# Performance work log

Hardware: AMD Instinct MI355X
Metric: run time of the kernel (lower is better)

## Reference

```python
import jax, jax.numpy as jnp
import numpy as np

B, L, D, T, NL = 64, 512, 512, 5000, 2


def setup_inputs() -> dict:
    key = jax.random.key(0)
    k1, k2, k3, k4 = jax.random.split(key, 4)
    enc_output = jax.random.normal(k1, (B, L, D), dtype=jnp.float32)
    # stands in for the row/col-normalized tag co-occurrence matrix (values in [0, 0.01])
    ui_adj = jax.random.uniform(k2, (T, T), dtype=jnp.float32) * 0.01
    # one GCN weight matrix per layer in the layer_stack
    Ws = jax.random.normal(k3, (NL, D, D), dtype=jnp.float32) / np.sqrt(D).astype(np.float32)
    # event ids are 1-indexed in the original (it indexes with e - 1)
    event_type = jax.random.randint(k4, (B, L), 1, T + 1, dtype=jnp.int64)
    slf_attn_mask = jnp.zeros((B, L, L), dtype=bool)
    non_pad_mask = jnp.ones((B, L), dtype=bool)
    return {"enc_output": enc_output, "ui_adj": ui_adj, "Ws": Ws,
            "event_type": event_type, "slf_attn_mask": slf_attn_mask,
            "non_pad_mask": non_pad_mask}


def reference(enc_output, ui_adj, Ws, event_type, slf_attn_mask, non_pad_mask):
    # --- batched per-sample adjacency gather (replaces the Python loop) ---
    idx = event_type - 1                                   # [B, L] 0-indexed
    sub = ui_adj[idx[:, :, None], idx[:, None, :]]         # [B, L, L] = ui_adj[e-1,:][:, e-1]
    diag = ui_adj[idx, idx]                                # [B, L]   = ui_adj[e-1, e-1]
    adj = sub + diag[:, None, :]                           # vector broadcasts across rows, as in torch
    # --- GNN layer stack (hGCN layer ~ relu(A @ X @ W)) ---
    x = enc_output
    for l in range(Ws.shape[0]):                           # small fixed n_layers loop
        x = jax.nn.relu(jnp.einsum('bij,bjd->bid', adj, x) @ Ws[l])
    # --- mean pool over sequence ---
    return x.mean(axis=1)                                  # [B, D]
```

## Files before the change

kernel.cpp:

```cpp
#include <hip/hip_runtime.h>

typedef unsigned short u16;
typedef unsigned int u32;
typedef __bf16 bf16x8 __attribute__((ext_vector_type(8)));
typedef float f32x4 __attribute__((ext_vector_type(4)));
typedef int i32x4 __attribute__((ext_vector_type(4)));
typedef u32 u32x2 __attribute__((ext_vector_type(2)));
typedef u32 u32x4 __attribute__((ext_vector_type(4)));

#define T_ 5000
#define CAP 96

__device__ __forceinline__ u16 f2bf(float f) {
  u32 u = __float_as_uint(f);
  u += 0x7fffu + ((u >> 16) & 1u);
  return (u16)(u >> 16);
}
__device__ __forceinline__ float bf2f(u32 bits16) {
  return __uint_as_float(bits16 << 16);
}

__device__ __forceinline__ void gload_lds16(const u16* g, u16* l) {
  __builtin_amdgcn_global_load_lds(
      (__attribute__((address_space(1))) void*)(u16*)g,
      (__attribute__((address_space(3))) void*)l, 16, 0, 0);
}

__device__ __forceinline__ u32 lds_off(const void* p) {
  return (u32)(uintptr_t)(__attribute__((address_space(3))) const void*)p;
}

__global__ void transpose_cast(const float* __restrict__ src, u16* __restrict__ dst) {
  __shared__ float tile[32][33];
  const int tx = threadIdx.x, ty = threadIdx.y;
  const int a0 = blockIdx.x * 32;
  const int b0 = blockIdx.y * 32;
  const size_t zoff = (size_t)blockIdx.z * (512 * 512);
  const float* s = src + zoff;
  u16* d = dst + zoff;
#pragma unroll
  for (int r = 0; r < 4; ++r)
    tile[ty + r * 8][tx] = s[(size_t)(a0 + ty + r * 8) * 512 + b0 + tx];
  __syncthreads();
#pragma unroll
  for (int r = 0; r < 4; ++r)
    d[(size_t)(b0 + ty + r * 8) * 512 + a0 + tx] = f2bf(tile[tx][ty + r * 8]);
}

__global__ void zero_k(int* __restrict__ cnt) {
  const int t = blockIdx.x * 256 + threadIdx.x;
  if (t < 5001) cnt[t] = 0;
}

__global__ void fill_k(const int* __restrict__ ev, const float* __restrict__ ui,
                       int2* __restrict__ cd, int* __restrict__ cnt,
                       int* __restrict__ list, int* __restrict__ ovf) {
  const int t = blockIdx.x * 256 + threadIdx.x;
  const int r = ev[t] - 1;
  int2 v;
  v.x = r;
  v.y = __float_as_int(ui[(size_t)r * (T_ + 1)]);
  cd[t] = v;
  const int pos = atomicAdd(&cnt[r], 1);
  if (pos < CAP) list[r * CAP + pos] = t;
  else { const int o = atomicAdd(&cnt[5000], 1); ovf[o] = t; }
}

__global__ __launch_bounds__(256)
void grow_gather(const float* __restrict__ ui, const int2* __restrict__ cd,
                 const int* __restrict__ cnt, const int* __restrict__ list,
                 u16* __restrict__ adj) {
  const int r = blockIdx.x;
  int c = cnt[r];
  if (c <= 0) return;
  if (c > CAP) c = CAP;
  __shared__ float row[5000];
  const float* __restrict__ src = ui + (size_t)r * T_;
  for (int t = threadIdx.x; t < 1250; t += 256)
    *(float4*)&row[t * 4] = *(const float4*)&src[t * 4];
  __syncthreads();
  const int j = threadIdx.x * 2;
  const int lb = r * CAP;
  int q = 0;
  for (; q + 2 <= c; q += 2) {
    const int t0 = list[lb + q], t1 = list[lb + q + 1];
    const int b0 = (t0 >> 9) << 9, b1 = (t1 >> 9) << 9;
    const int4 p0 = *(const int4*)&cd[b0 + j];
    const int4 p1 = *(const int4*)&cd[b1 + j];
    const u32 pk0 = (u32)f2bf(row[p0.x] + __int_as_float(p0.y)) |
                    ((u32)f2bf(row[p0.z] + __int_as_float(p0.w)) << 16);
    const u32 pk1 = (u32)f2bf(row[p1.x] + __int_as_float(p1.y)) |
                    ((u32)f2bf(row[p1.z] + __int_as_float(p1.w)) << 16);
    *(u32*)&adj[(size_t)t0 * 512 + j] = pk0;
    *(u32*)&adj[(size_t)t1 * 512 + j] = pk1;
  }
  if (q < c) {
    const int t0 = list[lb + q];
    const int b0 = (t0 >> 9) << 9;
    const int4 p0 = *(const int4*)&cd[b0 + j];
    const u32 pk0 = (u32)f2bf(row[p0.x] + __int_as_float(p0.y)) |
                    ((u32)f2bf(row[p0.z] + __int_as_float(p0.w)) << 16);
    *(u32*)&adj[(size_t)t0 * 512 + j] = pk0;
  }
}

__global__ void ovf_gather(const float* __restrict__ ui, const int2* __restrict__ cd,
                           const int* __restrict__ cnt, const int* __restrict__ ovf,
                           u16* __restrict__ adj) {
  const int n = cnt[5000];
  for (int q = blockIdx.x; q < n; q += gridDim.x) {
    const int t = ovf[q];
    const int base = (t >> 9) << 9;
    const long r = (long)cd[t].x;
    const float* __restrict__ row = ui + r * (long)T_;
    const int j = threadIdx.x * 2;
    const int4 p = *(const int4*)&cd[base + j];
    const u32 pk = (u32)f2bf(row[p.x] + __int_as_float(p.y)) |
                   ((u32)f2bf(row[p.z] + __int_as_float(p.w)) << 16);
    *(u32*)&adj[(size_t)t * 512 + j] = pk;
  }
}

template <int MODE, int BSRC>
__global__ __launch_bounds__(512, 2)
void gemm256(const u16* __restrict__ A, const void* __restrict__ Bv,
             u16* __restrict__ C, size_t strideA, size_t strideB, size_t strideC,
             float* __restrict__ P) {
  extern __shared__ u16 smem[];
  const int tid = threadIdx.x;
  const int lane = tid & 63;
  const int w = tid >> 6;
  const int wm = w >> 2, wn = w & 3;
  const int chunk = gridDim.x >> 3;
  const int wg = blockIdx.x;
  const int mapped = (wg & 7) * chunk + (wg >> 3);
  const int batch = mapped >> 2;
  const int tm = (mapped >> 1) & 1, tn = mapped & 1;
  const int m0 = tm << 8, n0 = tn << 8;
  const u16* __restrict__ Ab = A + (size_t)batch * strideA;

  const u16* gA[2];
  u32 ldA[2];
#pragma unroll
  for (int r = 0; r < 2; ++r) {
    const int c = r * 512 + tid;
    const int L = c * 16;
    const int pp = L >> 7;
    const int off = (L & 127) ^ ((pp & 7) << 4);
    const int m = pp * 2 + (off >> 6);
    const int kb = off & 63;
    gA[r] = Ab + (size_t)(m0 + m) * 512 + (kb >> 1);
    ldA[r] = (u32)((r * 512 + w * 64) * 8);
  }

  const u16* gB[2] = {nullptr, nullptr};
  u32 ldB[2] = {0, 0};
  if (BSRC == 0) {
    const u16* __restrict__ Bb = (const u16*)Bv + (size_t)batch * strideB;
#pragma unroll
    for (int r = 0; r < 2; ++r) {
      const int c = r * 512 + tid;
      const int L = c * 16;
      const int pp = L >> 7;
      const int off = (L & 127) ^ ((pp & 7) << 4);
      const int m = pp * 2 + (off >> 6);
      const int kb = off & 63;
      gB[r] = Bb + (size_t)(n0 + m) * 512 + (kb >> 1);
      ldB[r] = (u32)(32768 + (r * 512 + w * 64) * 8);
    }
  }

  const int dp = tid & 127;
  const int lq = tid >> 7;
  unsigned long long encB = 0;
  u32 boff0 = 0;
  u32x2 bs0[8], bs1[8];
  if (BSRC == 1) {
    encB = (unsigned long long)(uintptr_t)((const float*)Bv + (size_t)batch * strideB);
    boff0 = (u32)(((lq * 8) * 512 + n0 + dp * 2) * 4);
  }

#define BLOAD(t, S)                                                          \
  {                                                                          \
    const u32 ob = boff0 + (u32)(t) * 65536u;                                \
    _Pragma("unroll") for (int i = 0; i < 8; ++i)                            \
        asm volatile("global_load_dwordx2 %0, %1, %2"                        \
                     : "=v"(S[i])                                            \
                     : "v"(ob + (u32)i * 2048u), "s"(encB));                 \
  }

#define CONVERT_B(S)                                                         \
  {                                                                          \
    u32 wrd0[4], wrd1[4];                                                    \
    _Pragma("unroll") for (int jj = 0; jj < 4; ++jj) {                       \
      asm("v_cvt_pk_bf16_f32 %0, %1, %2"                                     \
          : "=v"(wrd0[jj]) : "v"(S[2 * jj].x), "v"(S[2 * jj + 1].x));        \
      asm("v_cvt_pk_bf16_f32 %0, %1, %2"                                     \
          : "=v"(wrd1[jj]) : "v"(S[2 * jj].y), "v"(S[2 * jj + 1].y));        \
    }                                                                        \
    const u32 by0 = (u32)dp * 128u + ((((u32)lq * 16u)) ^ (((u32)dp & 7u) << 4)); \
    const u32 by1 = (u32)dp * 128u + ((64u | ((u32)lq * 16u)) ^ (((u32)dp & 7u) << 4)); \
    u32x4 v0, v1;                                                            \
    v0.x = wrd0[0]; v0.y = wrd0[1]; v0.z = wrd0[2]; v0.w = wrd0[3];          \
    v1.x = wrd1[0]; v1.y = wrd1[1]; v1.z = wrd1[2]; v1.w = wrd1[3];          \
    *(u32x4*)((char*)smem + 65536 + by0) = v0;                               \
    *(u32x4*)((char*)smem + 65536 + by1) = v1;                               \
  }

  const int lr = lane & 15;
  const int kb = (lane >> 4) << 4;
  u32 aOff[8], bOff[4];
#pragma unroll
  for (int m = 0; m < 8; ++m) {
    const int row = wm * 128 + m * 16 + lr;
    aOff[m] = (u32)((row >> 1) * 128 + ((((row & 1) << 6) | kb) ^ (((row >> 1) & 7) << 4)));
  }
#pragma unroll
  for (int n = 0; n < 4; ++n) {
    const int row = wn * 64 + n * 16 + lr;
    bOff[n] = (u32)(65536 + (row >> 1) * 128 + ((((row & 1) << 6) | kb) ^ (((row >> 1) & 7) << 4)));
  }
  const u32 ldsBase = lds_off(smem);

  f32x4 acc[8][4] = {};

  auto stageA = [&](int t) {
    const u32 bo = (u32)(t & 3) * 8192;
#pragma unroll
    for (int r = 0; r < 2; ++r) gload_lds16(gA[r] + t * 32, smem + bo + ldA[r]);
  };
  auto stageB0 = [&](int t) {
    const u32 bo = (u32)(t & 3) * 8192;
#pragma unroll
    for (int r = 0; r < 2; ++r) gload_lds16(gB[r] + t * 32, smem + bo + ldB[r]);
  };

  if (BSRC == 0) {
    stageA(0); stageB0(0); stageA(1); stageB0(1); stageA(2); stageB0(2);
  } else {
    stageA(0); stageA(1); stageA(2);
    BLOAD(0, bs0); BLOAD(1, bs1);
  }

#pragma unroll
  for (int t = 0; t < 16; ++t) {
    if (BSRC == 0) {
      if (t <= 13)      asm volatile("s_waitcnt vmcnt(8)" ::: "memory");
      else if (t == 14) asm volatile("s_waitcnt vmcnt(4)" ::: "memory");
      else              asm volatile("s_waitcnt vmcnt(0)" ::: "memory");
      __builtin_amdgcn_sched_barrier(0);
      if (t + 3 < 16) { stageA(t + 3); stageB0(t + 3); }
      asm volatile("" ::: "memory");
      __builtin_amdgcn_s_barrier();
      asm volatile("" ::: "memory");
    } else {
      if (t == 0)              asm volatile("s_waitcnt vmcnt(8)" ::: "memory");
      else if (t <= 13)        asm volatile("s_waitcnt vmcnt(10)" ::: "memory");
      else if (t == 14)        asm volatile("s_waitcnt vmcnt(8)" ::: "memory");
      else                     asm volatile("s_waitcnt vmcnt(0)" ::: "memory");
      __builtin_amdgcn_sched_barrier(0);
      if (t & 1) { CONVERT_B(bs1); } else { CONVERT_B(bs0); }
      if (t + 3 < 16) stageA(t + 3);
      if (t + 2 < 16) { if (t & 1) { BLOAD(t + 2, bs1); } else { BLOAD(t + 2, bs0); } }
      asm volatile("s_waitcnt lgkmcnt(0)" ::: "memory");
      __builtin_amdgcn_s_barrier();
      asm volatile("" ::: "memory");
    }

    const u32 abase = ldsBase + (u32)(t & 3) * 16384;
    const u32 bbase = (BSRC == 0) ? (ldsBase + (u32)(t & 3) * 16384) : ldsBase;
    i32x4 araw[8], braw[4];
#pragma unroll
    for (int m = 0; m < 8; ++m)
      asm volatile("ds_read_b128 %0, %1" : "=v"(araw[m]) : "v"(abase + aOff[m]));
#pragma unroll
    for (int n = 0; n < 4; ++n)
      asm volatile("ds_read_b128 %0, %1" : "=v"(braw[n]) : "v"(bbase + bOff[n]));
    asm volatile("s_waitcnt lgkmcnt(0)" ::: "memory");
    __builtin_amdgcn_sched_barrier(0);

    __builtin_amdgcn_s_setprio(1);
#pragma unroll
    for (int m = 0; m < 8; ++m)
#pragma unroll
      for (int n = 0; n < 4; ++n)
        acc[m][n] = __builtin_amdgcn_mfma_f32_16x16x32_bf16(
            __builtin_bit_cast(bf16x8, araw[m]),
            __builtin_bit_cast(bf16x8, braw[n]), acc[m][n], 0, 0, 0);
    __builtin_amdgcn_s_setprio(0);
    asm volatile("" ::: "memory");
    __builtin_amdgcn_s_barrier();
    __builtin_amdgcn_sched_barrier(0);
  }
#undef BLOAD
#undef CONVERT_B

  u16* Cb = C + (size_t)batch * strideC;
  if (MODE == 0) {
#pragma unroll
    for (int m = 0; m < 8; ++m) {
      const int row = m0 + wm * 128 + m * 16 + (lane >> 4) * 4;
#pragma unroll
      for (int n = 0; n < 4; ++n) {
        const int col = n0 + wn * 64 + n * 16 + (lane & 15);
        const f32x4 v = acc[m][n];
#pragma unroll
        for (int j = 0; j < 4; ++j)
          Cb[(size_t)(row + j) * 512 + col] = f2bf(v[j]);
      }
    }
  } else if (MODE == 1) {
#pragma unroll
    for (int m = 0; m < 8; ++m) {
      const int i = m0 + wm * 128 + m * 16 + (lane >> 4) * 4;
#pragma unroll
      for (int n = 0; n < 4; ++n) {
        const int d = n0 + wn * 64 + n * 16 + (lane & 15);
        const f32x4 v = acc[m][n];
        uint2 p;
        p.x = (u32)f2bf(fmaxf(v[0], 0.f)) | ((u32)f2bf(fmaxf(v[1], 0.f)) << 16);
        p.y = (u32)f2bf(fmaxf(v[2], 0.f)) | ((u32)f2bf(fmaxf(v[3], 0.f)) << 16);
        *(uint2*)&Cb[(size_t)d * 512 + i] = p;
      }
    }
  } else {
    const int slot = tm * 2 + wm;
#pragma unroll
    for (int n = 0; n < 4; ++n) {
      float s = 0.f;
#pragma unroll
      for (int m = 0; m < 8; ++m) {
        const f32x4 v = acc[m][n];
#pragma unroll
        for (int j = 0; j < 4; ++j) s += fmaxf(v[j], 0.f);
      }
      s += __shfl_xor(s, 16);
      s += __shfl_xor(s, 32);
      if ((lane >> 4) == 0) {
        const int d = n0 + wn * 64 + n * 16 + lane;
        P[((size_t)batch * 4 + slot) * 512 + d] = s;
      }
    }
  }
}

__global__ void reduce_mean(const float* __restrict__ P, float* __restrict__ out) {
  const int t = blockIdx.x * 256 + threadIdx.x;
  const int b = t >> 9, d = t & 511;
  float s = 0.f;
#pragma unroll
  for (int q = 0; q < 4; ++q) s += P[((size_t)b * 4 + q) * 512 + d];
  out[t] = s * (1.0f / 512.0f);
}

extern "C" void kernel_launch(void* const* d_in, const int* in_sizes, int n_in,
                              void* d_out, int out_size, void* d_ws, size_t ws_size,
                              hipStream_t stream) {
  const float* enc = (const float*)d_in[0];
  const float* ui  = (const float*)d_in[1];
  const float* Ws  = (const float*)d_in[2];
  const int*   ev  = (const int*)d_in[3];
  float* out = (float*)d_out;

  char* ws = (char*)d_ws;
  const size_t SLAB = (size_t)64 * 512 * 512 * 2;
  u16* adj  = (u16*)(ws);
  u16* tbuf = (u16*)(ws + SLAB);
  u16* xb   = (u16*)(ws + 2 * SLAB);
  char* p = ws + 3 * SLAB;
  u16* wst  = (u16*)p;  p += (size_t)2 * 512 * 512 * 2;
  int2* cd  = (int2*)p; p += (size_t)32768 * 8;
  int* cnt  = (int*)p;  p += 5008 * 4;
  int* list = (int*)p;  p += (size_t)5000 * CAP * 4;
  int* ovf  = (int*)p;  p += (size_t)32768 * 4;
  float* P  = (float*)p;

  const size_t PS = (size_t)512 * 512;
  const size_t SMEM0 = 131072;
  const size_t SMEM1 = 81920;
  (void)hipFuncSetAttribute(reinterpret_cast<const void*>(gemm256<0, 1>),
                            hipFuncAttributeMaxDynamicSharedMemorySize, (int)SMEM1);
  (void)hipFuncSetAttribute(reinterpret_cast<const void*>(gemm256<1, 0>),
                            hipFuncAttributeMaxDynamicSharedMemorySize, (int)SMEM0);
  (void)hipFuncSetAttribute(reinterpret_cast<const void*>(gemm256<0, 0>),
                            hipFuncAttributeMaxDynamicSharedMemorySize, (int)SMEM0);
  (void)hipFuncSetAttribute(reinterpret_cast<const void*>(gemm256<2, 0>),
                            hipFuncAttributeMaxDynamicSharedMemorySize, (int)SMEM0);

  zero_k<<<20, 256, 0, stream>>>(cnt);
  fill_k<<<128, 256, 0, stream>>>(ev, ui, cd, cnt, list, ovf);
  transpose_cast<<<dim3(16, 16, 2), dim3(32, 8), 0, stream>>>(Ws, wst);
  grow_gather<<<5000, 256, 0, stream>>>(ui, cd, cnt, list, adj);
  ovf_gather<<<8, 256, 0, stream>>>(ui, cd, cnt, ovf, adj);
  gemm256<0, 1><<<256, 512, SMEM1, stream>>>(adj, enc, tbuf, PS, PS, PS, nullptr);
  gemm256<1, 0><<<256, 512, SMEM0, stream>>>(tbuf, wst, xb, PS, 0, PS, nullptr);
  gemm256<0, 0><<<256, 512, SMEM0, stream>>>(adj, xb, tbuf, PS, PS, PS, nullptr);
  gemm256<2, 0><<<256, 512, SMEM0, stream>>>(tbuf, wst + PS, nullptr, PS, 0, 0, P);
  reduce_mean<<<128, 256, 0, stream>>>(P, out);
}
```

Before: 141.1 us.

## Add transposed-output GEMM mode and merge small setup kernels

```diff
diff --git a/kernel.cpp b/kernel.cpp
--- a/kernel.cpp
+++ b/kernel.cpp
@@ -16,9 +16,6 @@
   u += 0x7fffu + ((u >> 16) & 1u);
   return (u16)(u >> 16);
 }
-__device__ __forceinline__ float bf2f(u32 bits16) {
-  return __uint_as_float(bits16 << 16);
-}
 
 __device__ __forceinline__ void gload_lds16(const u16* g, u16* l) {
   __builtin_amdgcn_global_load_lds(
@@ -30,7 +27,13 @@
   return (u32)(uintptr_t)(__attribute__((address_space(3))) const void*)p;
 }
 
-__global__ void transpose_cast(const float* __restrict__ src, u16* __restrict__ dst) {
+__device__ __forceinline__ u32 swz(int row, int kb) {
+  return (u32)((row >> 1) * 128 +
+               ((((row & 1) << 6) | kb) ^ (((row >> 1) & 7) << 4)));
+}
+
+__global__ void prep_k(const float* __restrict__ src, u16* __restrict__ dst,
+                       int* __restrict__ cnt) {
   __shared__ float tile[32][33];
   const int tx = threadIdx.x, ty = threadIdx.y;
   const int a0 = blockIdx.x * 32;
@@ -41,15 +44,12 @@
 #pragma unroll
   for (int r = 0; r < 4; ++r)
     tile[ty + r * 8][tx] = s[(size_t)(a0 + ty + r * 8) * 512 + b0 + tx];
+  const int gid = ((blockIdx.z * 16 + blockIdx.y) * 16 + blockIdx.x) * 256 + ty * 32 + tx;
+  if (gid < 5008) cnt[gid] = 0;
   __syncthreads();
 #pragma unroll
   for (int r = 0; r < 4; ++r)
     d[(size_t)(b0 + ty + r * 8) * 512 + a0 + tx] = f2bf(tile[tx][ty + r * 8]);
-}
-
-__global__ void zero_k(int* __restrict__ cnt) {
-  const int t = blockIdx.x * 256 + threadIdx.x;
-  if (t < 5001) cnt[t] = 0;
 }
 
 __global__ void fill_k(const int* __restrict__ ev, const float* __restrict__ ui,
@@ -69,55 +69,58 @@
 __global__ __launch_bounds__(256)
 void grow_gather(const float* __restrict__ ui, const int2* __restrict__ cd,
                  const int* __restrict__ cnt, const int* __restrict__ list,
-                 u16* __restrict__ adj) {
+                 const int* __restrict__ ovf, u16* __restrict__ adj) {
+  __shared__ float row[5000];
+  __shared__ int lst[CAP];
   const int r = blockIdx.x;
   int c = cnt[r];
-  if (c <= 0) return;
   if (c > CAP) c = CAP;
-  __shared__ float row[5000];
-  const float* __restrict__ src = ui + (size_t)r * T_;
-  for (int t = threadIdx.x; t < 1250; t += 256)
-    *(float4*)&row[t * 4] = *(const float4*)&src[t * 4];
-  __syncthreads();
   const int j = threadIdx.x * 2;
-  const int lb = r * CAP;
-  int q = 0;
-  for (; q + 2 <= c; q += 2) {
-    const int t0 = list[lb + q], t1 = list[lb + q + 1];
-    const int b0 = (t0 >> 9) << 9, b1 = (t1 >> 9) << 9;
-    const int4 p0 = *(const int4*)&cd[b0 + j];
-    const int4 p1 = *(const int4*)&cd[b1 + j];
-    const u32 pk0 = (u32)f2bf(row[p0.x] + __int_as_float(p0.y)) |
-                    ((u32)f2bf(row[p0.z] + __int_as_float(p0.w)) << 16);
-    const u32 pk1 = (u32)f2bf(row[p1.x] + __int_as_float(p1.y)) |
-                    ((u32)f2bf(row[p1.z] + __int_as_float(p1.w)) << 16);
-    *(u32*)&adj[(size_t)t0 * 512 + j] = pk0;
-    *(u32*)&adj[(size_t)t1 * 512 + j] = pk1;
-  }
-  if (q < c) {
-    const int t0 = list[lb + q];
-    const int b0 = (t0 >> 9) << 9;
-    const int4 p0 = *(const int4*)&cd[b0 + j];
-    const u32 pk0 = (u32)f2bf(row[p0.x] + __int_as_float(p0.y)) |
-                    ((u32)f2bf(row[p0.z] + __int_as_float(p0.w)) << 16);
-    *(u32*)&adj[(size_t)t0 * 512 + j] = pk0;
-  }
-}
-
-__global__ void ovf_gather(const float* __restrict__ ui, const int2* __restrict__ cd,
-                           const int* __restrict__ cnt, const int* __restrict__ ovf,
-                           u16* __restrict__ adj) {
-  const int n = cnt[5000];
-  for (int q = blockIdx.x; q < n; q += gridDim.x) {
-    const int t = ovf[q];
-    const int base = (t >> 9) << 9;
-    const long r = (long)cd[t].x;
-    const float* __restrict__ row = ui + r * (long)T_;
-    const int j = threadIdx.x * 2;
-    const int4 p = *(const int4*)&cd[base + j];
-    const u32 pk = (u32)f2bf(row[p.x] + __int_as_float(p.y)) |
-                   ((u32)f2bf(row[p.z] + __int_as_float(p.w)) << 16);
-    *(u32*)&adj[(size_t)t * 512 + j] = pk;
+  if (c > 0) {
+    const float* __restrict__ src = ui + (size_t)r * T_;
+    for (int t = threadIdx.x; t < 1250; t += 256)
+      *(float4*)&row[t * 4] = *(const float4*)&src[t * 4];
+    if (threadIdx.x < c) lst[threadIdx.x] = list[r * CAP + threadIdx.x];
+    __syncthreads();
+    int q = 0;
+    for (; q + 4 <= c; q += 4) {
+      const int t0 = lst[q], t1 = lst[q + 1], t2 = lst[q + 2], t3 = lst[q + 3];
+      const int4 p0 = *(const int4*)&cd[((t0 >> 9) << 9) + j];
+      const int4 p1 = *(const int4*)&cd[((t1 >> 9) << 9) + j];
+      const int4 p2 = *(const int4*)&cd[((t2 >> 9) << 9) + j];
+      const int4 p3 = *(const int4*)&cd[((t3 >> 9) << 9) + j];
+      const u32 k0 = (u32)f2bf(row[p0.x] + __int_as_float(p0.y)) |
+                     ((u32)f2bf(row[p0.z] + __int_as_float(p0.w)) << 16);
+      const u32 k1 = (u32)f2bf(row[p1.x] + __int_as_float(p1.y)) |
+                     ((u32)f2bf(row[p1.z] + __int_as_float(p1.w)) << 16);
+      const u32 k2 = (u32)f2bf(row[p2.x] + __int_as_float(p2.y)) |
+                     ((u32)f2bf(row[p2.z] + __int_as_float(p2.w)) << 16);
+      const u32 k3 = (u32)f2bf(row[p3.x] + __int_as_float(p3.y)) |
+                     ((u32)f2bf(row[p3.z] + __int_as_float(p3.w)) << 16);
+      *(u32*)&adj[(size_t)t0 * 512 + j] = k0;
+      *(u32*)&adj[(size_t)t1 * 512 + j] = k1;
+      *(u32*)&adj[(size_t)t2 * 512 + j] = k2;
+      *(u32*)&adj[(size_t)t3 * 512 + j] = k3;
+    }
+    for (; q < c; ++q) {
+      const int t0 = lst[q];
+      const int4 p0 = *(const int4*)&cd[((t0 >> 9) << 9) + j];
+      const u32 k0 = (u32)f2bf(row[p0.x] + __int_as_float(p0.y)) |
+                     ((u32)f2bf(row[p0.z] + __int_as_float(p0.w)) << 16);
+      *(u32*)&adj[(size_t)t0 * 512 + j] = k0;
+    }
+  }
+  if (r < 8) {
+    const int n = cnt[5000];
+    for (int q = r; q < n; q += 8) {
+      const int t = ovf[q];
+      const long rr = (long)cd[t].x;
+      const float* __restrict__ rp = ui + rr * (long)T_;
+      const int4 p = *(const int4*)&cd[((t >> 9) << 9) + j];
+      const u32 pk = (u32)f2bf(rp[p.x] + __int_as_float(p.y)) |
+                     ((u32)f2bf(rp[p.z] + __int_as_float(p.w)) << 16);
+      *(u32*)&adj[(size_t)t * 512 + j] = pk;
+    }
   }
 }
 
@@ -137,6 +140,8 @@
   const int batch = mapped >> 2;
   const int tm = (mapped >> 1) & 1, tn = mapped & 1;
   const int m0 = tm << 8, n0 = tn << 8;
+  const int r0base = (MODE == 3) ? n0 : m0;
+  const int r1base = (MODE == 3) ? m0 : n0;
   const u16* __restrict__ Ab = A + (size_t)batch * strideA;
 
   const u16* gA[2];
@@ -149,7 +154,7 @@
     const int off = (L & 127) ^ ((pp & 7) << 4);
     const int m = pp * 2 + (off >> 6);
     const int kb = off & 63;
-    gA[r] = Ab + (size_t)(m0 + m) * 512 + (kb >> 1);
+    gA[r] = Ab + (size_t)(r0base + m) * 512 + (kb >> 1);
     ldA[r] = (u32)((r * 512 + w * 64) * 8);
   }
 
@@ -165,7 +170,7 @@
       const int off = (L & 127) ^ ((pp & 7) << 4);
       const int m = pp * 2 + (off >> 6);
       const int kb = off & 63;
-      gB[r] = Bb + (size_t)(n0 + m) * 512 + (kb >> 1);
+      gB[r] = Bb + (size_t)(r1base + m) * 512 + (kb >> 1);
       ldB[r] = (u32)(32768 + (r * 512 + w * 64) * 8);
     }
   }
@@ -177,7 +182,7 @@
   u32x2 bs0[8], bs1[8];
   if (BSRC == 1) {
     encB = (unsigned long long)(uintptr_t)((const float*)Bv + (size_t)batch * strideB);
-    boff0 = (u32)(((lq * 8) * 512 + n0 + dp * 2) * 4);
+    boff0 = (u32)(((lq * 8) * 512 + r1base + dp * 2) * 4);
   }
 
 #define BLOAD(t, S)                                                          \
@@ -208,18 +213,12 @@
   }
 
   const int lr = lane & 15;
-  const int kb = (lane >> 4) << 4;
-  u32 aOff[8], bOff[4];
-#pragma unroll
-  for (int m = 0; m < 8; ++m) {
-    const int row = wm * 128 + m * 16 + lr;
-    aOff[m] = (u32)((row >> 1) * 128 + ((((row & 1) << 6) | kb) ^ (((row >> 1) & 7) << 4)));
-  }
-#pragma unroll
-  for (int n = 0; n < 4; ++n) {
-    const int row = wn * 64 + n * 16 + lr;
-    bOff[n] = (u32)(65536 + (row >> 1) * 128 + ((((row & 1) << 6) | kb) ^ (((row >> 1) & 7) << 4)));
-  }
+  const int kbB = (lane >> 4) << 4;
+  u32 fOff8[8], fOff4[4];
+#pragma unroll
+  for (int m = 0; m < 8; ++m) fOff8[m] = swz(wm * 128 + m * 16 + lr, kbB);
+#pragma unroll
+  for (int n = 0; n < 4; ++n) fOff4[n] = swz(wn * 64 + n * 16 + lr, kbB);
   const u32 ldsBase = lds_off(smem);
 
   f32x4 acc[8][4] = {};
@@ -267,15 +266,17 @@
       asm volatile("" ::: "memory");
     }
 
-    const u32 abase = ldsBase + (u32)(t & 3) * 16384;
-    const u32 bbase = (BSRC == 0) ? (ldsBase + (u32)(t & 3) * 16384) : ldsBase;
+    const u32 c0 = ldsBase + (u32)(t & 3) * 16384;
+    const u32 c1 = ldsBase + 65536u + (BSRC == 0 ? (u32)(t & 3) * 16384 : 0u);
+    const u32 base8 = (MODE == 3) ? c1 : c0;
+    const u32 base4 = (MODE == 3) ? c0 : c1;
     i32x4 araw[8], braw[4];
 #pragma unroll
     for (int m = 0; m < 8; ++m)
-      asm volatile("ds_read_b128 %0, %1" : "=v"(araw[m]) : "v"(abase + aOff[m]));
+      asm volatile("ds_read_b128 %0, %1" : "=v"(araw[m]) : "v"(base8 + fOff8[m]));
 #pragma unroll
     for (int n = 0; n < 4; ++n)
-      asm volatile("ds_read_b128 %0, %1" : "=v"(braw[n]) : "v"(bbase + bOff[n]));
+      asm volatile("ds_read_b128 %0, %1" : "=v"(braw[n]) : "v"(base4 + fOff4[n]));
     asm volatile("s_waitcnt lgkmcnt(0)" ::: "memory");
     __builtin_amdgcn_sched_barrier(0);
 
@@ -296,20 +297,7 @@
 #undef CONVERT_B
 
   u16* Cb = C + (size_t)batch * strideC;
-  if (MODE == 0) {
-#pragma unroll
-    for (int m = 0; m < 8; ++m) {
-      const int row = m0 + wm * 128 + m * 16 + (lane >> 4) * 4;
-#pragma unroll
-      for (int n = 0; n < 4; ++n) {
-        const int col = n0 + wn * 64 + n * 16 + (lane & 15);
-        const f32x4 v = acc[m][n];
-#pragma unroll
-        for (int j = 0; j < 4; ++j)
-          Cb[(size_t)(row + j) * 512 + col] = f2bf(v[j]);
-      }
-    }
-  } else if (MODE == 1) {
+  if (MODE == 1) {
 #pragma unroll
     for (int m = 0; m < 8; ++m) {
       const int i = m0 + wm * 128 + m * 16 + (lane >> 4) * 4;
@@ -323,7 +311,7 @@
         *(uint2*)&Cb[(size_t)d * 512 + i] = p;
       }
     }
-  } else {
+  } else if (MODE == 2) {
     const int slot = tm * 2 + wm;
 #pragma unroll
     for (int n = 0; n < 4; ++n) {
@@ -339,6 +327,20 @@
       if ((lane >> 4) == 0) {
         const int d = n0 + wn * 64 + n * 16 + lane;
         P[((size_t)batch * 4 + slot) * 512 + d] = s;
+      }
+    }
+  } else {
+#pragma unroll
+    for (int m = 0; m < 8; ++m) {
+      const int dd = m0 + wm * 128 + m * 16 + (lane >> 4) * 4;
+#pragma unroll
+      for (int n = 0; n < 4; ++n) {
+        const int ii = n0 + wn * 64 + n * 16 + (lane & 15);
+        const f32x4 v = acc[m][n];
+        uint2 p;
+        p.x = (u32)f2bf(v[0]) | ((u32)f2bf(v[1]) << 16);
+        p.y = (u32)f2bf(v[2]) | ((u32)f2bf(v[3]) << 16);
+        *(uint2*)&Cb[(size_t)ii * 512 + dd] = p;
       }
     }
   }
@@ -378,23 +380,21 @@
   const size_t PS = (size_t)512 * 512;
   const size_t SMEM0 = 131072;
   const size_t SMEM1 = 81920;
-  (void)hipFuncSetAttribute(reinterpret_cast<const void*>(gemm256<0, 1>),
+  (void)hipFuncSetAttribute(reinterpret_cast<const void*>(gemm256<3, 1>),
                             hipFuncAttributeMaxDynamicSharedMemorySize, (int)SMEM1);
   (void)hipFuncSetAttribute(reinterpret_cast<const void*>(gemm256<1, 0>),
                             hipFuncAttributeMaxDynamicSharedMemorySize, (int)SMEM0);
-  (void)hipFuncSetAttribute(reinterpret_cast<const void*>(gemm256<0, 0>),
+  (void)hipFuncSetAttribute(reinterpret_cast<const void*>(gemm256<3, 0>),
                             hipFuncAttributeMaxDynamicSharedMemorySize, (int)SMEM0);
   (void)hipFuncSetAttribute(reinterpret_cast<const void*>(gemm256<2, 0>),
                             hipFuncAttributeMaxDynamicSharedMemorySize, (int)SMEM0);
 
-  zero_k<<<20, 256, 0, stream>>>(cnt);
+  prep_k<<<dim3(16, 16, 2), dim3(32, 8), 0, stream>>>(Ws, wst, cnt);
   fill_k<<<128, 256, 0, stream>>>(ev, ui, cd, cnt, list, ovf);
-  transpose_cast<<<dim3(16, 16, 2), dim3(32, 8), 0, stream>>>(Ws, wst);
-  grow_gather<<<5000, 256, 0, stream>>>(ui, cd, cnt, list, adj);
-  ovf_gather<<<8, 256, 0, stream>>>(ui, cd, cnt, ovf, adj);
-  gemm256<0, 1><<<256, 512, SMEM1, stream>>>(adj, enc, tbuf, PS, PS, PS, nullptr);
+  grow_gather<<<5000, 256, 0, stream>>>(ui, cd, cnt, list, ovf, adj);
+  gemm256<3, 1><<<256, 512, SMEM1, stream>>>(adj, enc, tbuf, PS, PS, PS, nullptr);
   gemm256<1, 0><<<256, 512, SMEM0, stream>>>(tbuf, wst, xb, PS, 0, PS, nullptr);
-  gemm256<0, 0><<<256, 512, SMEM0, stream>>>(adj, xb, tbuf, PS, PS, PS, nullptr);
+  gemm256<3, 0><<<256, 512, SMEM0, stream>>>(adj, xb, tbuf, PS, PS, PS, nullptr);
   gemm256<2, 0><<<256, 512, SMEM0, stream>>>(tbuf, wst + PS, nullptr, PS, 0, 0, P);
   reduce_mean<<<128, 256, 0, stream>>>(P, out);
 }
```

New measurement: 142.6 us. Within noise of the previous version (+1.1%).
